# Performance work log

Measured on AMD Instinct MI355X. Metric: run time of the kernel, lower is better.

Reference implementation:

```python
import jax, jax.numpy as jnp
import numpy as np

R = 32  # reduced channel dim = outplane // reduction
TRI_I, TRI_J = np.triu_indices(R)  # static upper-triangle indices (528 pairs)


def setup_inputs() -> dict:
    key = jax.random.key(0)
    k1, k2, k3 = jax.random.split(key, 3)
    B, Cin, H, W = 8, 256, 96, 96
    Cout = 256
    tri = R * (R + 1) // 2  # 528
    x = jax.random.normal(k1, (B, Cin, H, W), dtype=jnp.float32)
    # 1x1 conv weights stored as [out, in] matrices
    w_reduce = jax.random.normal(k2, (R, Cin), dtype=jnp.float32) * (1.0 / np.sqrt(Cin))
    w_recover = jax.random.normal(k3, (Cout, tri), dtype=jnp.float32) * (1.0 / np.sqrt(tri))
    return {"x": x, "w_reduce": w_reduce, "w_recover": w_recover}


def reference(x, w_reduce, w_recover):
    # reduce: 1x1 conv (no bias): [B,Cin,H,W] -> [B,R,H,W]
    out = jnp.einsum('bchw,rc->brhw', x, w_reduce)
    # per-pixel outer product, but only the upper-triangle entries:
    # bilinear[b,i,j,h,w] = out[b,i,h,w] * out[b,j,h,w]; gather (i,j) in triu
    i = jnp.asarray(TRI_I)
    j = jnp.asarray(TRI_J)
    up = out[:, i, :, :] * out[:, j, :, :]  # [B, 528, H, W]
    # channelRecover: 1x1 conv 528 -> Cout
    y = jnp.einsum('bthw,ot->bohw', up, w_recover)
    # signed sqrt
    return jnp.sign(y) * jnp.sqrt(jnp.abs(y) + 1e-6)
```

## Files before the change

### kernel.cpp

```cpp
#include <hip/hip_runtime.h>
#include <hip/hip_bf16.h>
#include <math.h>

#define HW     9216
#define CIN    256
#define RCH    32
#define NTRI   528
#define COUT   256
#define NB     8
#define W16ROW 544
#define UPROW  296

typedef _Float16 f16x8 __attribute__((ext_vector_type(8)));
typedef float    f32x4 __attribute__((ext_vector_type(4)));

struct TriTab { unsigned char i[544]; unsigned char j[544]; };
constexpr TriTab make_tri() {
  TriTab t{};
  int ii = 0, jj = 0;
  for (int k = 0; k < 544; ++k) {
    if (k < NTRI) {
      t.i[k] = (unsigned char)ii; t.j[k] = (unsigned char)jj;
      if (++jj == 32) { ++ii; jj = ii; }
    } else { t.i[k] = 0; t.j[k] = 0; }
  }
  return t;
}
constexpr TriTab TRI = make_tri();

template<int TQ, int HALF>
__device__ __forceinline__ void build_up(const float (&o)[RCH], _Float16* rowp) {
  constexpr int NG  = HALF ? 8 : 9;
  constexpr int TLB = TQ * (HALF ? 64 : 72);
  constexpr int TB  = HALF ? 288 : 0;
#pragma unroll
  for (int g = 0; g < NG; ++g) {
    f16x8 v;
#pragma unroll
    for (int s = 0; s < 8; ++s) {
      const int tl = TLB + g * 8 + s;
      const int t  = TB + tl;
      float f = (t < NTRI) ? o[TRI.i[t]] * o[TRI.j[t]] : 0.0f;
      v[s] = (_Float16)f;
    }
    *(f16x8*)&rowp[TLB + g * 8] = v;
  }
}

template<int HALF>
__device__ __forceinline__ void build_dispatch(int wv, const float (&o)[RCH],
                                               _Float16* rowp) {
  if (wv == 0)      build_up<0, HALF>(o, rowp);
  else if (wv == 1) build_up<1, HALF>(o, rowp);
  else if (wv == 2) build_up<2, HALF>(o, rowp);
  else              build_up<3, HALF>(o, rowp);
}

__global__ __launch_bounds__(256) void convert_kernel(
    const float* __restrict__ w_reduce, const float* __restrict__ w_recover,
    _Float16* __restrict__ w16, _Float16* __restrict__ wr16h,
    _Float16* __restrict__ wr16l) {
  const int bx = blockIdx.x;
  const int tid = threadIdx.x;
  if (bx < COUT) {
    for (int t = tid; t < W16ROW; t += 256) {
      float f = (t < NTRI) ? w_recover[(size_t)bx * NTRI + t] : 0.0f;
      w16[(size_t)bx * W16ROW + t] = (_Float16)f;
    }
  } else {
    int e = (bx - COUT) * 512 + tid;
#pragma unroll
    for (int k = 0; k < 2; ++k, e += 256) {
      float f = w_reduce[e];
      _Float16 h = (_Float16)f;
      wr16h[e] = h;
      wr16l[e] = (_Float16)(f - (float)h);
    }
  }
}

__global__ __launch_bounds__(256, 3) void fused_kernel(
    const float* __restrict__ x, const _Float16* __restrict__ w16,
    const _Float16* __restrict__ wr16h, const _Float16* __restrict__ wr16l,
    float* __restrict__ y) {
  __shared__ float outS[RCH * 68];
  __shared__ __align__(16) _Float16 upS[64 * UPROW];

  const int tid  = threadIdx.x;
  const int bx   = blockIdx.x;
  const int b    = bx / 144;
  const int p0   = (bx - b * 144) * 64;
  const int wv   = tid >> 6;
  const int lane = tid & 63;
  const int ml   = lane & 15;
  const int q    = lane >> 4;

  {
    f32x4 g1acc[2];
#pragma unroll
    for (int mt = 0; mt < 2; ++mt)
#pragma unroll
      for (int r2 = 0; r2 < 4; ++r2) g1acc[mt][r2] = 0.0f;

    const float* xb = x + (size_t)b * CIN * HW + p0 + wv * 16 + ml;
#pragma unroll
    for (int ch = 0; ch < 8; ++ch) {
      const int c0 = ch * 32;
      float xv[8];
#pragma unroll
      for (int s = 0; s < 8; ++s)
        xv[s] = xb[(size_t)(c0 + q * 8 + s) * HW];
      f16x8 bh, bl;
#pragma unroll
      for (int s = 0; s < 8; ++s) {
        _Float16 h = (_Float16)xv[s];
        bh[s] = h;
        bl[s] = (_Float16)(xv[s] - (float)h);
      }
#pragma unroll
      for (int mt = 0; mt < 2; ++mt) {
        const int off = (mt * 16 + ml) * CIN + c0 + q * 8;
        f16x8 ah = *(const f16x8*)&wr16h[off];
        f16x8 al = *(const f16x8*)&wr16l[off];
        g1acc[mt] = __builtin_amdgcn_mfma_f32_16x16x32_f16(ah, bh, g1acc[mt], 0, 0, 0);
        g1acc[mt] = __builtin_amdgcn_mfma_f32_16x16x32_f16(al, bh, g1acc[mt], 0, 0, 0);
        g1acc[mt] = __builtin_amdgcn_mfma_f32_16x16x32_f16(ah, bl, g1acc[mt], 0, 0, 0);
      }
    }
#pragma unroll
    for (int mt = 0; mt < 2; ++mt)
#pragma unroll
      for (int reg = 0; reg < 4; ++reg)
        outS[(mt * 16 + q * 4 + reg) * 68 + wv * 16 + ml] = g1acc[mt][reg];
  }
  __syncthreads();

  f32x4 acc[4][4];
#pragma unroll
  for (int mi = 0; mi < 4; ++mi)
#pragma unroll
    for (int ni = 0; ni < 4; ++ni)
#pragma unroll
      for (int r2 = 0; r2 < 4; ++r2) acc[mi][ni][r2] = 0.0f;

  _Float16* rowp = &upS[lane * UPROW];

  {
    float o[RCH];
#pragma unroll
    for (int r = 0; r < RCH; ++r) o[r] = outS[r * 68 + lane];
    build_dispatch<0>(wv, o, rowp);
  }
  __syncthreads();
#pragma unroll
  for (int c = 0; c < 9; ++c) {
    const int t0 = c * 32;
    f16x8 afr[4];
#pragma unroll
    for (int mi = 0; mi < 4; ++mi)
      afr[mi] = *(const f16x8*)&w16[(size_t)(wv * 64 + mi * 16 + ml) * W16ROW + t0 + q * 8];
    f16x8 bfr[4];
#pragma unroll
    for (int ni = 0; ni < 4; ++ni)
      bfr[ni] = *(const f16x8*)&upS[(ni * 16 + ml) * UPROW + t0 + q * 8];
#pragma unroll
    for (int mi = 0; mi < 4; ++mi)
#pragma unroll
      for (int ni = 0; ni < 4; ++ni)
        acc[mi][ni] = __builtin_amdgcn_mfma_f32_16x16x32_f16(afr[mi], bfr[ni], acc[mi][ni], 0, 0, 0);
  }
  __syncthreads();

  {
    float o[RCH];
#pragma unroll
    for (int r = 0; r < RCH; ++r) o[r] = outS[r * 68 + lane];
    build_dispatch<1>(wv, o, rowp);
  }
  __syncthreads();
#pragma unroll
  for (int c = 0; c < 8; ++c) {
    const int t0l = c * 32;
    const int t0g = 288 + c * 32;
    f16x8 afr[4];
#pragma unroll
    for (int mi = 0; mi < 4; ++mi)
      afr[mi] = *(const f16x8*)&w16[(size_t)(wv * 64 + mi * 16 + ml) * W16ROW + t0g + q * 8];
    f16x8 bfr[4];
#pragma unroll
    for (int ni = 0; ni < 4; ++ni)
      bfr[ni] = *(const f16x8*)&upS[(ni * 16 + ml) * UPROW + t0l + q * 8];
#pragma unroll
    for (int mi = 0; mi < 4; ++mi)
#pragma unroll
      for (int ni = 0; ni < 4; ++ni)
        acc[mi][ni] = __builtin_amdgcn_mfma_f32_16x16x32_f16(afr[mi], bfr[ni], acc[mi][ni], 0, 0, 0);
  }

#pragma unroll
  for (int mi = 0; mi < 4; ++mi) {
#pragma unroll
    for (int reg = 0; reg < 4; ++reg) {
      const int o = wv * 64 + mi * 16 + q * 4 + reg;
      float* yrow = y + ((size_t)(b * COUT + o)) * HW + p0 + ml;
#pragma unroll
      for (int ni = 0; ni < 4; ++ni) {
        float v = acc[mi][ni][reg];
        float s = sqrtf(fabsf(v) + 1e-6f);
        yrow[ni * 16] = v > 0.0f ? s : (v < 0.0f ? -s : 0.0f);
      }
    }
  }
}

extern "C" void kernel_launch(void* const* d_in, const int* in_sizes, int n_in,
                              void* d_out, int out_size, void* d_ws, size_t ws_size,
                              hipStream_t stream) {
  const float* x         = (const float*)d_in[0];
  const float* w_reduce  = (const float*)d_in[1];
  const float* w_recover = (const float*)d_in[2];
  float* y = (float*)d_out;

  _Float16* w16   = (_Float16*)d_ws;
  _Float16* wr16h = (_Float16*)((char*)d_ws + 278528);
  _Float16* wr16l = (_Float16*)((char*)d_ws + 278528 + 16384);

  convert_kernel<<<COUT + 16, 256, 0, stream>>>(w_reduce, w_recover, w16, wr16h, wr16l);
  fused_kernel<<<NB * (HW / 64), 256, 0, stream>>>(x, w16, wr16h, wr16l, y);
}
```

Before: 179.9 us.

## Split fused kernel work across 8 waves per block instead of 4

The block grows from 256 to 512 threads. Each wave now handles half as many output channels in the recover GEMM and one reduce tile in the first GEMM, and the upper-triangle product build is split into 8 slices of 4 halves. Per-thread accumulator state shrinks from 16 to 8 MFMA tiles, which lowers register pressure and should allow more waves in flight to hide the x loads and output stores. In exchange, each wave loads the shared up-tile B fragments with less reuse per load, and the smaller f16x4 LDS stores are less efficient.

Measured after the change: 187.5 us. +4.3%, slower.

```diff
diff --git a/kernel.cpp b/kernel.cpp
--- a/kernel.cpp
+++ b/kernel.cpp
@@ -12,6 +12,7 @@
 #define UPROW  296
 
 typedef _Float16 f16x8 __attribute__((ext_vector_type(8)));
+typedef _Float16 f16x4 __attribute__((ext_vector_type(4)));
 typedef float    f32x4 __attribute__((ext_vector_type(4)));
 
 struct TriTab { unsigned char i[544]; unsigned char j[544]; };
@@ -31,29 +32,35 @@
 template<int TQ, int HALF>
 __device__ __forceinline__ void build_up(const float (&o)[RCH], _Float16* rowp) {
   constexpr int NG  = HALF ? 8 : 9;
-  constexpr int TLB = TQ * (HALF ? 64 : 72);
+  constexpr int TLB = TQ * (HALF ? 32 : 36);
   constexpr int TB  = HALF ? 288 : 0;
 #pragma unroll
   for (int g = 0; g < NG; ++g) {
-    f16x8 v;
-#pragma unroll
-    for (int s = 0; s < 8; ++s) {
-      const int tl = TLB + g * 8 + s;
+    f16x4 v;
+#pragma unroll
+    for (int s = 0; s < 4; ++s) {
+      const int tl = TLB + g * 4 + s;
       const int t  = TB + tl;
       float f = (t < NTRI) ? o[TRI.i[t]] * o[TRI.j[t]] : 0.0f;
       v[s] = (_Float16)f;
     }
-    *(f16x8*)&rowp[TLB + g * 8] = v;
+    *(f16x4*)&rowp[TLB + g * 4] = v;
   }
 }
 
 template<int HALF>
 __device__ __forceinline__ void build_dispatch(int wv, const float (&o)[RCH],
                                                _Float16* rowp) {
-  if (wv == 0)      build_up<0, HALF>(o, rowp);
-  else if (wv == 1) build_up<1, HALF>(o, rowp);
-  else if (wv == 2) build_up<2, HALF>(o, rowp);
-  else              build_up<3, HALF>(o, rowp);
+  switch (wv) {
+    case 0: build_up<0, HALF>(o, rowp); break;
+    case 1: build_up<1, HALF>(o, rowp); break;
+    case 2: build_up<2, HALF>(o, rowp); break;
+    case 3: build_up<3, HALF>(o, rowp); break;
+    case 4: build_up<4, HALF>(o, rowp); break;
+    case 5: build_up<5, HALF>(o, rowp); break;
+    case 6: build_up<6, HALF>(o, rowp); break;
+    default: build_up<7, HALF>(o, rowp); break;
+  }
 }
 
 __global__ __launch_bounds__(256) void convert_kernel(
@@ -79,7 +86,7 @@
   }
 }
 
-__global__ __launch_bounds__(256, 3) void fused_kernel(
+__global__ __launch_bounds__(512, 4) void fused_kernel(
     const float* __restrict__ x, const _Float16* __restrict__ w16,
     const _Float16* __restrict__ wr16h, const _Float16* __restrict__ wr16l,
     float* __restrict__ y) {
@@ -94,15 +101,15 @@
   const int lane = tid & 63;
   const int ml   = lane & 15;
   const int q    = lane >> 4;
+  const int mt   = wv >> 2;
+  const int nt   = wv & 3;
 
   {
-    f32x4 g1acc[2];
-#pragma unroll
-    for (int mt = 0; mt < 2; ++mt)
-#pragma unroll
-      for (int r2 = 0; r2 < 4; ++r2) g1acc[mt][r2] = 0.0f;
-
-    const float* xb = x + (size_t)b * CIN * HW + p0 + wv * 16 + ml;
+    f32x4 g1acc;
+#pragma unroll
+    for (int r2 = 0; r2 < 4; ++r2) g1acc[r2] = 0.0f;
+
+    const float* xb = x + (size_t)b * CIN * HW + p0 + nt * 16 + ml;
 #pragma unroll
     for (int ch = 0; ch < 8; ++ch) {
       const int c0 = ch * 32;
@@ -117,27 +124,22 @@
         bh[s] = h;
         bl[s] = (_Float16)(xv[s] - (float)h);
       }
-#pragma unroll
-      for (int mt = 0; mt < 2; ++mt) {
-        const int off = (mt * 16 + ml) * CIN + c0 + q * 8;
-        f16x8 ah = *(const f16x8*)&wr16h[off];
-        f16x8 al = *(const f16x8*)&wr16l[off];
-        g1acc[mt] = __builtin_amdgcn_mfma_f32_16x16x32_f16(ah, bh, g1acc[mt], 0, 0, 0);
-        g1acc[mt] = __builtin_amdgcn_mfma_f32_16x16x32_f16(al, bh, g1acc[mt], 0, 0, 0);
-        g1acc[mt] = __builtin_amdgcn_mfma_f32_16x16x32_f16(ah, bl, g1acc[mt], 0, 0, 0);
-      }
-    }
-#pragma unroll
-    for (int mt = 0; mt < 2; ++mt)
-#pragma unroll
-      for (int reg = 0; reg < 4; ++reg)
-        outS[(mt * 16 + q * 4 + reg) * 68 + wv * 16 + ml] = g1acc[mt][reg];
-  }
-  __syncthreads();
-
-  f32x4 acc[4][4];
-#pragma unroll
-  for (int mi = 0; mi < 4; ++mi)
+      const int off = (mt * 16 + ml) * CIN + c0 + q * 8;
+      f16x8 ah = *(const f16x8*)&wr16h[off];
+      f16x8 al = *(const f16x8*)&wr16l[off];
+      g1acc = __builtin_amdgcn_mfma_f32_16x16x32_f16(ah, bh, g1acc, 0, 0, 0);
+      g1acc = __builtin_amdgcn_mfma_f32_16x16x32_f16(al, bh, g1acc, 0, 0, 0);
+      g1acc = __builtin_amdgcn_mfma_f32_16x16x32_f16(ah, bl, g1acc, 0, 0, 0);
+    }
+#pragma unroll
+    for (int reg = 0; reg < 4; ++reg)
+      outS[(mt * 16 + q * 4 + reg) * 68 + nt * 16 + ml] = g1acc[reg];
+  }
+  __syncthreads();
+
+  f32x4 acc[2][4];
+#pragma unroll
+  for (int mi = 0; mi < 2; ++mi)
 #pragma unroll
     for (int ni = 0; ni < 4; ++ni)
 #pragma unroll
@@ -155,16 +157,16 @@
 #pragma unroll
   for (int c = 0; c < 9; ++c) {
     const int t0 = c * 32;
-    f16x8 afr[4];
-#pragma unroll
-    for (int mi = 0; mi < 4; ++mi)
-      afr[mi] = *(const f16x8*)&w16[(size_t)(wv * 64 + mi * 16 + ml) * W16ROW + t0 + q * 8];
+    f16x8 afr[2];
+#pragma unroll
+    for (int mi = 0; mi < 2; ++mi)
+      afr[mi] = *(const f16x8*)&w16[(size_t)(wv * 32 + mi * 16 + ml) * W16ROW + t0 + q * 8];
     f16x8 bfr[4];
 #pragma unroll
     for (int ni = 0; ni < 4; ++ni)
       bfr[ni] = *(const f16x8*)&upS[(ni * 16 + ml) * UPROW + t0 + q * 8];
 #pragma unroll
-    for (int mi = 0; mi < 4; ++mi)
+    for (int mi = 0; mi < 2; ++mi)
 #pragma unroll
       for (int ni = 0; ni < 4; ++ni)
         acc[mi][ni] = __builtin_amdgcn_mfma_f32_16x16x32_f16(afr[mi], bfr[ni], acc[mi][ni], 0, 0, 0);
@@ -182,26 +184,26 @@
   for (int c = 0; c < 8; ++c) {
     const int t0l = c * 32;
     const int t0g = 288 + c * 32;
-    f16x8 afr[4];
-#pragma unroll
-    for (int mi = 0; mi < 4; ++mi)
-      afr[mi] = *(const f16x8*)&w16[(size_t)(wv * 64 + mi * 16 + ml) * W16ROW + t0g + q * 8];
+    f16x8 afr[2];
+#pragma unroll
+    for (int mi = 0; mi < 2; ++mi)
+      afr[mi] = *(const f16x8*)&w16[(size_t)(wv * 32 + mi * 16 + ml) * W16ROW + t0g + q * 8];
     f16x8 bfr[4];
 #pragma unroll
     for (int ni = 0; ni < 4; ++ni)
       bfr[ni] = *(const f16x8*)&upS[(ni * 16 + ml) * UPROW + t0l + q * 8];
 #pragma unroll
-    for (int mi = 0; mi < 4; ++mi)
+    for (int mi = 0; mi < 2; ++mi)
 #pragma unroll
       for (int ni = 0; ni < 4; ++ni)
         acc[mi][ni] = __builtin_amdgcn_mfma_f32_16x16x32_f16(afr[mi], bfr[ni], acc[mi][ni], 0, 0, 0);
   }
 
 #pragma unroll
-  for (int mi = 0; mi < 4; ++mi) {
+  for (int mi = 0; mi < 2; ++mi) {
 #pragma unroll
     for (int reg = 0; reg < 4; ++reg) {
-      const int o = wv * 64 + mi * 16 + q * 4 + reg;
+      const int o = wv * 32 + mi * 16 + q * 4 + reg;
       float* yrow = y + ((size_t)(b * COUT + o)) * HW + p0 + ml;
 #pragma unroll
       for (int ni = 0; ni < 4; ++ni) {
@@ -226,5 +228,5 @@
   _Float16* wr16l = (_Float16*)((char*)d_ws + 278528 + 16384);
 
   convert_kernel<<<COUT + 16, 256, 0, stream>>>(w_reduce, w_recover, w16, wr16h, wr16l);
-  fused_kernel<<<NB * (HW / 64), 256, 0, stream>>>(x, w16, wr16h, wr16l, y);
-}
+  fused_kernel<<<NB * (HW / 64), 512, 0, stream>>>(x, w16, wr16h, wr16l, y);
+}
```
